# Optimization experiments

Hardware: AMD Instinct MI355X
Metric: run time of the kernel (lower is better)

Reference implementation:

```python
import jax, jax.numpy as jnp
import numpy as np
import math

B, T, D, H = 4, 2048, 2048, 16
HD = D // H  # 128


def rotate_half(x):
    half = x.shape[-1] // 2
    return jnp.concatenate([-x[..., half:], x[..., :half]], axis=-1)


def apply_rope(x, cos, sin):
    # x: [B,H,T,hd]; cos/sin: [T,hd] -> broadcast over B,H
    return x * cos[None, None] + rotate_half(x) * sin[None, None]


def setup_inputs() -> dict:
    key = jax.random.key(0)
    ks = jax.random.split(key, 6)
    x = jax.random.normal(ks[0], (B, T, D), dtype=jnp.float32)
    # standard RoPE tables
    inv_freq = 1.0 / (10000.0 ** (np.arange(0, HD, 2, dtype=np.float32) / HD))
    freqs = np.arange(T, dtype=np.float32)[:, None] * inv_freq[None, :]  # [T, hd/2]
    emb = np.concatenate([freqs, freqs], axis=-1)  # [T, hd]
    cos = jnp.asarray(np.cos(emb))
    sin = jnp.asarray(np.sin(emb))
    # additive causal mask [T,T]: 0 on/below diagonal, -1e9 above
    mask = jnp.where(jnp.tril(jnp.ones((T, T), dtype=bool)), 0.0, -1e9).astype(jnp.float32)
    scale = 0.02
    Wq = scale * jax.random.normal(ks[1], (D, D), dtype=jnp.float32)
    Wk = scale * jax.random.normal(ks[2], (D, D), dtype=jnp.float32)
    Wv = scale * jax.random.normal(ks[3], (D, D), dtype=jnp.float32)
    Wo = scale * jax.random.normal(ks[4], (D, D), dtype=jnp.float32)
    return {"x": x, "cos": cos, "sin": sin, "mask": mask,
            "Wq": Wq, "Wk": Wk, "Wv": Wv, "Wo": Wo}


def reference(x, cos, sin, mask, Wq, Wk, Wv, Wo):
    b, t, d = x.shape

    def split_heads(y):  # [B,T,D] -> [B,H,T,hd]
        return y.reshape(b, t, H, HD).transpose(0, 2, 1, 3)

    # nn.Linear: y = x @ W.T
    Q = apply_rope(split_heads(jnp.einsum('btd,od->bto', x, Wq)), cos, sin)
    K = apply_rope(split_heads(jnp.einsum('btd,od->bto', x, Wk)), cos, sin)
    V = split_heads(jnp.einsum('btd,od->bto', x, Wv))

    scores = jnp.einsum('bhqd,bhkd->bhqk', Q, K) / math.sqrt(HD)
    scores = scores + mask  # [T,T] broadcasts over [B,H,T,T]
    weights = jax.nn.softmax(scores, axis=-1)
    out = jnp.einsum('bhqk,bhkd->bhqd', weights, V)
    out = out.transpose(0, 2, 1, 3).reshape(b, t, d)
    return jnp.einsum('btd,od->bto', out, Wo)
```

## Files before the change

kernel.cpp:

```cpp
#include <hip/hip_runtime.h>
#include <hip/hip_bf16.h>

#define DEV static __device__ __forceinline__

typedef __attribute__((ext_vector_type(8))) _Float16 half8;
typedef __attribute__((ext_vector_type(4))) float f32x4;

constexpr int Bc = 4, Tc = 2048, Dc = 2048, Hc = 16;

DEV ushort f2h(float f) { _Float16 h = (_Float16)f; return __builtin_bit_cast(ushort, h); }
DEV float  h2f(ushort u) { return (float)__builtin_bit_cast(_Float16, u); }
DEV uint pk2h(float a, float b) {
  return __builtin_bit_cast(uint, __builtin_amdgcn_cvt_pkrtz(a, b));
}

DEV f32x4 MFMA(half8 a, half8 b, f32x4 c) {
  return __builtin_amdgcn_mfma_f32_16x16x32_f16(a, b, c, 0, 0, 0);
}

DEV void async_cp16(void* lds, const void* g) {
  __builtin_amdgcn_global_load_lds((const __attribute__((address_space(1))) void*)g,
                                   (__attribute__((address_space(3))) void*)lds,
                                   16, 0, 0);
}

__global__ __launch_bounds__(256) void cvtall(const float* __restrict__ x,
                                              const float* __restrict__ w0,
                                              const float* __restrict__ w1,
                                              const float* __restrict__ w2,
                                              const float* __restrict__ w3,
                                              ushort* __restrict__ xb,
                                              ushort* __restrict__ wb) {
  const int blk = (int)blockIdx.x;
  if (blk < 16384) {
    const int i = blk * 256 + (int)threadIdx.x;
    const float4 v = ((const float4*)x)[i];
    ushort4 o;
    o.x = f2h(v.x); o.y = f2h(v.y); o.z = f2h(v.z); o.w = f2h(v.w);
    ((ushort4*)xb)[i] = o;
    return;
  }
  const int wblk = blk - 16384;
  const int wsel = wblk >> 12;
  const int i = (wblk & 4095) * 256 + (int)threadIdx.x;
  const float* in = (wsel == 0) ? w0 : (wsel == 1) ? w1 : (wsel == 2) ? w2 : w3;
  const float4 v = ((const float4*)in)[i];
  ushort4 o;
  o.x = f2h(v.x); o.y = f2h(v.y); o.z = f2h(v.z); o.w = f2h(v.w);
  int row = i >> 9;
  const int cidx = i & 511;
  if (wsel < 2) {
    const int h = row >> 7, fr = row & 127;
    const int s_ = fr >> 6, j = fr & 63;
    row = h * 128 + (j >> 4) * 32 + s_ * 16 + (j & 15);
  }
  ((ushort4*)wb)[((size_t)wsel << 20) + row * 512 + cidx] = o;
}

__global__ __launch_bounds__(512, 2) void gemmqkv(const ushort* __restrict__ A,
                                                  const ushort* __restrict__ Bw,
                                                  ushort* __restrict__ Cq,
                                                  const float* __restrict__ cs,
                                                  const float* __restrict__ sn) {
  __shared__ ushort As[4][256 * 32];
  __shared__ ushort Bs[4][256 * 32];
  const int tid = threadIdx.x;
  const int lane = tid & 63, wid = tid >> 6;
  const int g = lane >> 4, q16 = lane & 15;
  const int wm = wid >> 2, wn = wid & 3;

  const int flat = (int)blockIdx.x;
  const int xcd = flat & 7, idx = flat >> 3;
  const int bm = xcd * 4 + (idx & 3);
  const int bn = idx >> 2;
  const ushort* Ab = A + (size_t)bm * 256 * Dc;
  const ushort* Bb = Bw + (size_t)bn * 256 * Dc;

#define STAGE1(KT, BUF, PH) do {                                               \
    const int pass_ = (PH) & 1;                                                \
    const int c_ = pass_ * 512 + tid;                                          \
    const int row_ = c_ >> 2, gl_ = c_ & 3;                                    \
    const int col_ = (KT) * 32 + ((gl_ ^ ((row_ >> 1) & 3)) << 3);             \
    if ((PH) < 2)                                                              \
      async_cp16(&As[BUF][(pass_ * 512 + wid * 64) * 8],                       \
                 Ab + (size_t)row_ * Dc + col_);                               \
    else                                                                       \
      async_cp16(&Bs[BUF][(pass_ * 512 + wid * 64) * 8],                       \
                 Bb + (size_t)row_ * Dc + col_);                               \
  } while (0)

  f32x4 acc[8][4] = {};

  for (int tt = 0; tt < 3; ++tt) {
    STAGE1(tt, tt, 0); STAGE1(tt, tt, 1);
    STAGE1(tt, tt, 2); STAGE1(tt, tt, 3);
  }

  const int sgz = (g ^ ((q16 >> 1) & 3)) << 3;

#pragma unroll 1
  for (int t = 0; t < 64; ++t) {
    const int sb = (t + 3) & 3;
    const bool st = (t + 3) < 64;
    const ushort* Asb = As[t & 3];
    const ushort* Bsb = Bs[t & 3];

    if (t + 2 < 64)      asm volatile("s_waitcnt vmcnt(8)" ::: "memory");
    else if (t + 1 < 64) asm volatile("s_waitcnt vmcnt(4)" ::: "memory");
    else                 asm volatile("s_waitcnt vmcnt(0)" ::: "memory");
    __builtin_amdgcn_s_barrier();
    __builtin_amdgcn_sched_barrier(0);

    half8 af0[4], af1[4], bf[4];
#pragma unroll
    for (int nf = 0; nf < 4; ++nf) {
      const int r = wn * 64 + nf * 16 + q16;
      bf[nf] = *(const half8*)&Bsb[r * 32 + sgz];
    }
#pragma unroll
    for (int mf = 0; mf < 4; ++mf) {
      const int r = wm * 128 + mf * 16 + q16;
      af0[mf] = *(const half8*)&Asb[r * 32 + sgz];
    }
#pragma unroll
    for (int mf = 0; mf < 4; ++mf) {
      const int r = wm * 128 + 64 + mf * 16 + q16;
      af1[mf] = *(const half8*)&Asb[r * 32 + sgz];
    }
    if (st) { STAGE1(t + 3, sb, 0); STAGE1(t + 3, sb, 1);
              STAGE1(t + 3, sb, 2); STAGE1(t + 3, sb, 3); }

    __builtin_amdgcn_s_setprio(1);
#pragma unroll
    for (int mf = 0; mf < 4; ++mf)
#pragma unroll
      for (int nf = 0; nf < 4; ++nf)
        acc[mf][nf] = MFMA(af0[mf], bf[nf], acc[mf][nf]);
#pragma unroll
    for (int mf = 0; mf < 4; ++mf)
#pragma unroll
      for (int nf = 0; nf < 4; ++nf)
        acc[4 + mf][nf] = MFMA(af1[mf], bf[nf], acc[4 + mf][nf]);
    __builtin_amdgcn_s_setprio(0);
  }
#undef STAGE1

  ushort* C = Cq + (size_t)(bn >> 3) * ((size_t)8192 * Dc);
  const int bn8 = bn & 7;
  const int m00 = bm * 256 + wm * 128 + g * 4;
  const int n0 = bn8 * 256 + wn * 64 + q16;

  if (bn < 16) {
#pragma unroll
    for (int mf = 0; mf < 8; ++mf)
#pragma unroll
      for (int p = 0; p < 2; ++p) {
        const int j = ((wn & 1) * 2 + p) * 16 + q16;
#pragma unroll
        for (int r = 0; r < 4; ++r) {
          const int m = m00 + mf * 16 + r;
          const int t = m & (Tc - 1);
          const float c = cs[t * 128 + j];
          const float s_ = sn[t * 128 + j];
          const float lo = acc[mf][2 * p][r];
          const float hi = acc[mf][2 * p + 1][r];
          C[(size_t)m * Dc + n0 + (2 * p) * 16] = f2h(lo * c - hi * s_);
          C[(size_t)m * Dc + n0 + (2 * p + 1) * 16] = f2h(hi * c + lo * s_);
        }
      }
  } else {
#pragma unroll
    for (int mf = 0; mf < 8; ++mf)
#pragma unroll
      for (int nf = 0; nf < 4; ++nf) {
        const int m0 = m00 + mf * 16;
        const int n = n0 + nf * 16;
#pragma unroll
        for (int r = 0; r < 4; ++r)
          C[(size_t)(m0 + r) * Dc + n] = f2h(acc[mf][nf][r]);
      }
  }
}

template <typename OutT>
__global__ __launch_bounds__(512, 2) void gemm256(const ushort* __restrict__ A,
                                                  const ushort* __restrict__ Bw,
                                                  OutT* __restrict__ C) {
  __shared__ ushort As[4][256 * 32];
  __shared__ ushort Bs[4][256 * 32];
  const int tid = threadIdx.x;
  const int lane = tid & 63, wid = tid >> 6;
  const int g = lane >> 4, q16 = lane & 15;
  const int wm = wid >> 2, wn = wid & 3;

  const int flat = (int)blockIdx.x;
  const int xcd = flat & 7, idx = flat >> 3;
  const int bm = xcd * 4 + (idx & 3);
  const int bn = idx >> 2;
  const ushort* Ab = A + (size_t)bm * 256 * Dc;
  const ushort* Bb = Bw + (size_t)bn * 256 * Dc;

#define STAGE1(KT, BUF, PH) do {                                               \
    const int pass_ = (PH) & 1;                                                \
    const int c_ = pass_ * 512 + tid;                                          \
    const int row_ = c_ >> 2, gl_ = c_ & 3;                                    \
    const int col_ = (KT) * 32 + ((gl_ ^ ((row_ >> 1) & 3)) << 3);             \
    if ((PH) < 2)                                                              \
      async_cp16(&As[BUF][(pass_ * 512 + wid * 64) * 8],                       \
                 Ab + (size_t)row_ * Dc + col_);                               \
    else                                                                       \
      async_cp16(&Bs[BUF][(pass_ * 512 + wid * 64) * 8],                       \
                 Bb + (size_t)row_ * Dc + col_);                               \
  } while (0)

  f32x4 acc[8][4] = {};

  for (int tt = 0; tt < 3; ++tt) {
    STAGE1(tt, tt, 0); STAGE1(tt, tt, 1);
    STAGE1(tt, tt, 2); STAGE1(tt, tt, 3);
  }

  const int sgz = (g ^ ((q16 >> 1) & 3)) << 3;

#pragma unroll 1
  for (int t = 0; t < 64; ++t) {
    const int sb = (t + 3) & 3;
    const bool st = (t + 3) < 64;
    const ushort* Asb = As[t & 3];
    const ushort* Bsb = Bs[t & 3];

    if (t + 2 < 64)      asm volatile("s_waitcnt vmcnt(8)" ::: "memory");
    else if (t + 1 < 64) asm volatile("s_waitcnt vmcnt(4)" ::: "memory");
    else                 asm volatile("s_waitcnt vmcnt(0)" ::: "memory");
    __builtin_amdgcn_s_barrier();
    __builtin_amdgcn_sched_barrier(0);

    half8 af0[4], af1[4], bf[4];
#pragma unroll
    for (int nf = 0; nf < 4; ++nf) {
      const int r = wn * 64 + nf * 16 + q16;
      bf[nf] = *(const half8*)&Bsb[r * 32 + sgz];
    }
#pragma unroll
    for (int mf = 0; mf < 4; ++mf) {
      const int r = wm * 128 + mf * 16 + q16;
      af0[mf] = *(const half8*)&Asb[r * 32 + sgz];
    }
#pragma unroll
    for (int mf = 0; mf < 4; ++mf) {
      const int r = wm * 128 + 64 + mf * 16 + q16;
      af1[mf] = *(const half8*)&Asb[r * 32 + sgz];
    }
    if (st) { STAGE1(t + 3, sb, 0); STAGE1(t + 3, sb, 1);
              STAGE1(t + 3, sb, 2); STAGE1(t + 3, sb, 3); }

    __builtin_amdgcn_s_setprio(1);
#pragma unroll
    for (int mf = 0; mf < 4; ++mf)
#pragma unroll
      for (int nf = 0; nf < 4; ++nf)
        acc[mf][nf] = MFMA(af0[mf], bf[nf], acc[mf][nf]);
#pragma unroll
    for (int mf = 0; mf < 4; ++mf)
#pragma unroll
      for (int nf = 0; nf < 4; ++nf)
        acc[4 + mf][nf] = MFMA(af1[mf], bf[nf], acc[4 + mf][nf]);
    __builtin_amdgcn_s_setprio(0);
  }
#undef STAGE1

  const int m00 = bm * 256 + wm * 128 + g * 4;
  const int n0 = bn * 256 + wn * 64 + q16;
#pragma unroll
  for (int mf = 0; mf < 8; ++mf)
#pragma unroll
    for (int nf = 0; nf < 4; ++nf) {
      const int m0 = m00 + mf * 16;
      const int n = n0 + nf * 16;
#pragma unroll
      for (int r = 0; r < 4; ++r) {
        const float v = acc[mf][nf][r];
        if constexpr (sizeof(OutT) == 2)
          C[(size_t)(m0 + r) * Dc + n] = (OutT)f2h(v);
        else
          C[(size_t)(m0 + r) * Dc + n] = (OutT)v;
      }
    }
}

__global__ __launch_bounds__(512, 2) void attn(const ushort* __restrict__ Q,
                                               const ushort* __restrict__ K,
                                               const ushort* __restrict__ V,
                                               ushort* __restrict__ O) {
  __shared__ ushort Ks[2][64 * 128];
  __shared__ ushort Vt[2][128 * 64];

  const int tid = threadIdx.x;
  const int lane = tid & 63, wid = tid >> 6;
  const int g = lane >> 4, q16 = lane & 15;

  const int flat = (int)(blockIdx.x + 4 * blockIdx.y);
  const int xcd = flat & 7, idx = flat >> 3;
  const int bh = xcd + 8 * (idx & 7);
  const int pr = idx >> 3;

  const int b = bh >> 4, h = bh & 15;
  const size_t headbase = ((size_t)b * Tc * Hc + h) * 128;
  const float SCL2 = 0.12751743f;

  const int vdc = (wid & 3) * 4 + (lane & 3);
  const int vkvp = (wid >> 2) * 16 + (lane >> 2);

  uint4 vreg[2];

#define ISSUEK(KT, BUF) do {                                                   \
    const ushort* Kb_ = K + headbase + (size_t)(KT) * 64 * Dc;                 \
    _Pragma("unroll") for (int i_ = 0; i_ < 2; ++i_) {                         \
      const int c_ = i_ * 512 + tid;                                           \
      const int kv_ = c_ >> 4, gl_ = c_ & 15;                                  \
      async_cp16(&Ks[BUF][(i_ * 512 + wid * 64) * 8],                          \
                 Kb_ + (size_t)kv_ * Dc + ((gl_ ^ (kv_ & 7)) << 3));           \
    }                                                                          \
  } while (0)

#define LOADV(KT) do {                                                         \
    const ushort* p0_ = V + headbase + (size_t)((KT) * 64 + 2 * vkvp) * Dc +   \
                        vdc * 8;                                               \
    vreg[0] = *(const uint4*)p0_;                                              \
    vreg[1] = *(const uint4*)(p0_ + Dc);                                       \
  } while (0)

#define WRITEV(BUF) do {                                                       \
    const ushort* e0_ = (const ushort*)&vreg[0];                               \
    const ushort* e1_ = (const ushort*)&vreg[1];                               \
    _Pragma("unroll") for (int j_ = 0; j_ < 8; ++j_) {                         \
      const int d_ = vdc * 8 + j_;                                             \
      const unsigned w_ = (unsigned)e0_[j_] | ((unsigned)e1_[j_] << 16);       \
      *(unsigned*)&Vt[BUF][(d_ * 64 + 2 * vkvp) ^ ((d_ & 7) << 3)] = w_;       \
    }                                                                          \
  } while (0)

#pragma unroll 1
  for (int half = 0; half < 2; ++half) {
    const int q0 = (half ? pr : 7 - pr) * 256;
    const int qrow = q0 + wid * 32;
    const int nt = q0 / 64 + 4;

    half8 qreg[2][4];
#pragma unroll
    for (int qf = 0; qf < 2; ++qf)
#pragma unroll
      for (int ds = 0; ds < 4; ++ds)
        qreg[qf][ds] = *(const half8*)(Q + headbase +
                       (size_t)(qrow + qf * 16 + q16) * Dc + ds * 32 + g * 8);

    f32x4 oacc[2][8] = {};
    float m_[2] = {-1e30f, -1e30f};
    float l_[2] = {0.f, 0.f};

    __builtin_amdgcn_s_barrier();
    __builtin_amdgcn_sched_barrier(0);
    ISSUEK(0, 0);
    LOADV(0);
    WRITEV(0);

#pragma unroll 1
    for (int kt = 0; kt < nt; ++kt) {
      const int cur = kt & 1;
      const int kv0 = kt * 64;
      asm volatile("s_waitcnt vmcnt(0) lgkmcnt(0)" ::: "memory");
      __builtin_amdgcn_s_barrier();
      __builtin_amdgcn_sched_barrier(0);
      if (kt + 1 < nt) {
        ISSUEK(kt + 1, cur ^ 1);
        LOADV(kt + 1);
      }

      if (kv0 <= qrow + 31) {
        const ushort* Ksb = Ks[cur];
        const ushort* Vtb = Vt[cur];
        f32x4 s[2][4] = {};
        __builtin_amdgcn_s_setprio(1);
#pragma unroll
        for (int ds = 0; ds < 4; ++ds) {
          half8 kf[4];
#pragma unroll
          for (int kvf = 0; kvf < 4; ++kvf) {
            const int kv = kvf * 16 + q16;
            kf[kvf] = *(const half8*)&Ksb[(kv * 128 + ds * 32 + g * 8) ^ ((kv & 7) << 3)];
          }
#pragma unroll
          for (int kvf = 0; kvf < 4; ++kvf)
#pragma unroll
            for (int qf = 0; qf < 2; ++qf)
              s[qf][kvf] = MFMA(kf[kvf], qreg[qf][ds], s[qf][kvf]);
        }
        __builtin_amdgcn_s_setprio(0);
        float pmax[2] = {-1e30f, -1e30f};
        if (kv0 + 63 > qrow) {
#pragma unroll
          for (int qf = 0; qf < 2; ++qf) {
            const int qg = qrow + qf * 16 + q16;
#pragma unroll
            for (int kvf = 0; kvf < 4; ++kvf)
#pragma unroll
              for (int r = 0; r < 4; ++r) {
                float v = s[qf][kvf][r];
                if ((kv0 + kvf * 16 + g * 4 + r) > qg) v = -1e30f;
                s[qf][kvf][r] = v;
                pmax[qf] = fmaxf(pmax[qf], v);
              }
          }
        } else {
#pragma unroll
          for (int qf = 0; qf < 2; ++qf)
#pragma unroll
            for (int kvf = 0; kvf < 4; ++kvf)
#pragma unroll
              for (int r = 0; r < 4; ++r)
                pmax[qf] = fmaxf(pmax[qf], s[qf][kvf][r]);
        }
#pragma unroll
        for (int qf = 0; qf < 2; ++qf) {
          pmax[qf] = fmaxf(pmax[qf], __shfl_xor(pmax[qf], 16));
          pmax[qf] = fmaxf(pmax[qf], __shfl_xor(pmax[qf], 32));
        }
        if (!__all((pmax[0] <= m_[0] + 16.f) & (pmax[1] <= m_[1] + 16.f))) {
#pragma unroll
          for (int qf = 0; qf < 2; ++qf) {
            const float mn2 = fmaxf(m_[qf], pmax[qf]);
            const float alpha = __builtin_exp2f((m_[qf] - mn2) * SCL2);
            m_[qf] = mn2;
            l_[qf] *= alpha;
#pragma unroll
            for (int df = 0; df < 8; ++df)
              oacc[qf][df] *= alpha;
          }
        }
        uint w[2][4][2];
#pragma unroll
        for (int qf = 0; qf < 2; ++qf) {
          const float mn = m_[qf];
          float lsum = 0.f;
#pragma unroll
          for (int kvf = 0; kvf < 4; ++kvf) {
            const float p0 = __builtin_exp2f((s[qf][kvf][0] - mn) * SCL2);
            const float p1 = __builtin_exp2f((s[qf][kvf][1] - mn) * SCL2);
            const float p2 = __builtin_exp2f((s[qf][kvf][2] - mn) * SCL2);
            const float p3 = __builtin_exp2f((s[qf][kvf][3] - mn) * SCL2);
            lsum += (p0 + p1) + (p2 + p3);
            w[qf][kvf][0] = pk2h(p0, p1);
            w[qf][kvf][1] = pk2h(p2, p3);
          }
          l_[qf] += lsum;
        }
        const bool ghi = g >= 2;
        const bool godd = (g & 1) != 0;
        half8 pb[2][2];
#pragma unroll
        for (int qf = 0; qf < 2; ++qf) {
          uint sA[2][2], sB[2][2];
#pragma unroll
          for (int c = 0; c < 2; ++c)
#pragma unroll
            for (int i = 0; i < 2; ++i) {
              sA[c][i] = ghi ? w[qf][2 * c + 1][i] : w[qf][2 * c][i];
              sB[c][i] = ghi ? w[qf][2 * c][i] : w[qf][2 * c + 1][i];
            }
          uint x16[2][2], x32[2][2], x48[2][2];
#pragma unroll
          for (int c = 0; c < 2; ++c)
#pragma unroll
            for (int i = 0; i < 2; ++i) {
              x16[c][i] = __shfl_xor(sA[c][i], 16);
              x32[c][i] = __shfl_xor(sB[c][i], 32);
              x48[c][i] = __shfl_xor(sB[c][i], 48);
            }
#pragma unroll
          for (int c = 0; c < 2; ++c) {
            uint4 t;
            t.x = godd ? (ghi ? x16[c][0] : x48[c][0]) : (ghi ? x32[c][0] : sA[c][0]);
            t.y = godd ? (ghi ? x16[c][1] : x48[c][1]) : (ghi ? x32[c][1] : sA[c][1]);
            t.z = godd ? (ghi ? sA[c][0] : x32[c][0]) : (ghi ? x48[c][0] : x16[c][0]);
            t.w = godd ? (ghi ? sA[c][1] : x32[c][1]) : (ghi ? x48[c][1] : x16[c][1]);
            pb[qf][c] = __builtin_bit_cast(half8, t);
          }
        }
        __builtin_amdgcn_s_setprio(1);
#pragma unroll
        for (int c = 0; c < 2; ++c) {
#pragma unroll
          for (int df = 0; df < 8; ++df) {
            const int d = df * 16 + q16;
            const half8 vf = *(const half8*)&Vtb[(d * 64 + c * 32 + g * 8) ^ ((d & 7) << 3)];
#pragma unroll
            for (int qf = 0; qf < 2; ++qf)
              oacc[qf][df] = MFMA(vf, pb[qf][c], oacc[qf][df]);
          }
        }
        __builtin_amdgcn_s_setprio(0);
      }

      if (kt + 1 < nt) WRITEV(cur ^ 1);
    }

#pragma unroll
    for (int qf = 0; qf < 2; ++qf) {
      float l = l_[qf];
      l += __shfl_xor(l, 16);
      l += __shfl_xor(l, 32);
      const float inv = 1.0f / l;
      const int t = qrow + qf * 16 + q16;
#pragma unroll
      for (int df = 0; df < 8; ++df) {
        const f32x4 v = oacc[qf][df];
        ushort4 o;
        o.x = f2h(v[0] * inv); o.y = f2h(v[1] * inv);
        o.z = f2h(v[2] * inv); o.w = f2h(v[3] * inv);
        *(ushort4*)(O + headbase + (size_t)t * Dc + df * 16 + g * 4) = o;
      }
    }
  }
#undef ISSUEK
#undef LOADV
#undef WRITEV
}

extern "C" void kernel_launch(void* const* d_in, const int* in_sizes, int n_in,
                              void* d_out, int out_size, void* d_ws, size_t ws_size,
                              hipStream_t stream) {
  (void)in_sizes; (void)n_in; (void)out_size; (void)ws_size;
  const float* x  = (const float*)d_in[0];
  const float* cs = (const float*)d_in[1];
  const float* sn = (const float*)d_in[2];
  const float* Wq = (const float*)d_in[4];
  const float* Wk = (const float*)d_in[5];
  const float* Wv = (const float*)d_in[6];
  const float* Wo = (const float*)d_in[7];
  float* out = (float*)d_out;

  char* ws = (char*)d_ws;
  const size_t MB = 1024 * 1024;
  ushort* xb  = (ushort*)(ws);
  ushort* wqb = (ushort*)(ws + 32 * MB);
  ushort* wob = (ushort*)(ws + 56 * MB);
  ushort* Qr  = (ushort*)(ws + 64 * MB);
  ushort* Kr  = (ushort*)(ws + 96 * MB);
  ushort* Vr  = (ushort*)(ws + 128 * MB);

  cvtall<<<32768, 256, 0, stream>>>(x, Wq, Wk, Wv, Wo, xb, wqb);

  gemmqkv<<<768, 512, 0, stream>>>(xb, wqb, Qr, cs, sn);

  attn<<<dim3(4, 64), 512, 0, stream>>>(Qr, Kr, Vr, xb);

  gemm256<float><<<256, 512, 0, stream>>>(xb, wob, out);
}
```

Baseline: 449.2 us.

## Switch GEMM mainloop to double-buffered BK=64 tiles with 8-way XOR swizzle

Both GEMM kernels (QKV projection and the generic 256x256 GEMM) change from a 4-stage BK=32 async pipeline to a 2-stage BK=64 pipeline. The LDS rows are now 64 halves wide with an 8-way XOR swizzle. Each iteration issues the next tile's loads up front, runs two k-substeps of MFMAs, then waits for all loads and barriers once. This halves the number of barriers and loop iterations. In exchange, prefetch depth drops to one tile and every iteration ends with a full vmcnt(0) wait, which can expose load latency.

```diff
diff --git a/kernel.cpp b/kernel.cpp
--- a/kernel.cpp
+++ b/kernel.cpp
@@ -62,8 +62,8 @@
                                                   ushort* __restrict__ Cq,
                                                   const float* __restrict__ cs,
                                                   const float* __restrict__ sn) {
-  __shared__ ushort As[4][256 * 32];
-  __shared__ ushort Bs[4][256 * 32];
+  __shared__ ushort As[2][256 * 64];
+  __shared__ ushort Bs[2][256 * 64];
   const int tid = threadIdx.x;
   const int lane = tid & 63, wid = tid >> 6;
   const int g = lane >> 4, q16 = lane & 15;
@@ -76,74 +76,87 @@
   const ushort* Ab = A + (size_t)bm * 256 * Dc;
   const ushort* Bb = Bw + (size_t)bn * 256 * Dc;
 
-#define STAGE1(KT, BUF, PH) do {                                               \
-    const int pass_ = (PH) & 1;                                                \
-    const int c_ = pass_ * 512 + tid;                                          \
-    const int row_ = c_ >> 2, gl_ = c_ & 3;                                    \
-    const int col_ = (KT) * 32 + ((gl_ ^ ((row_ >> 1) & 3)) << 3);             \
-    if ((PH) < 2)                                                              \
-      async_cp16(&As[BUF][(pass_ * 512 + wid * 64) * 8],                       \
+#define STAGE64(KT, BUF) do {                                                  \
+    _Pragma("unroll") for (int p_ = 0; p_ < 4; ++p_) {                         \
+      const int c_ = p_ * 512 + tid;                                           \
+      const int row_ = c_ >> 3, gl_ = c_ & 7;                                  \
+      const int col_ = (KT) * 64 + ((gl_ ^ (row_ & 7)) << 3);                  \
+      async_cp16(&As[BUF][(p_ * 512 + wid * 64) * 8],                          \
                  Ab + (size_t)row_ * Dc + col_);                               \
-    else                                                                       \
-      async_cp16(&Bs[BUF][(pass_ * 512 + wid * 64) * 8],                       \
+    }                                                                          \
+    _Pragma("unroll") for (int p_ = 0; p_ < 4; ++p_) {                         \
+      const int c_ = p_ * 512 + tid;                                           \
+      const int row_ = c_ >> 3, gl_ = c_ & 7;                                  \
+      const int col_ = (KT) * 64 + ((gl_ ^ (row_ & 7)) << 3);                  \
+      async_cp16(&Bs[BUF][(p_ * 512 + wid * 64) * 8],                          \
                  Bb + (size_t)row_ * Dc + col_);                               \
+    }                                                                          \
+  } while (0)
+
+#define READS64(BUF, KS) do {                                                  \
+    const ushort* Asb_ = As[BUF];                                              \
+    const ushort* Bsb_ = Bs[BUF];                                              \
+    _Pragma("unroll") for (int nf_ = 0; nf_ < 4; ++nf_) {                      \
+      const int r_ = wn * 64 + nf_ * 16 + q16;                                 \
+      bf[nf_] = *(const half8*)&Bsb_[r_ * 64 + ((((KS) * 4 + g) ^ (r_ & 7)) << 3)]; \
+    }                                                                          \
+    _Pragma("unroll") for (int mf_ = 0; mf_ < 4; ++mf_) {                      \
+      const int r_ = wm * 128 + mf_ * 16 + q16;                                \
+      af0[mf_] = *(const half8*)&Asb_[r_ * 64 + ((((KS) * 4 + g) ^ (r_ & 7)) << 3)]; \
+    }                                                                          \
+    _Pragma("unroll") for (int mf_ = 0; mf_ < 4; ++mf_) {                      \
+      const int r_ = wm * 128 + 64 + mf_ * 16 + q16;                           \
+      af1[mf_] = *(const half8*)&Asb_[r_ * 64 + ((((KS) * 4 + g) ^ (r_ & 7)) << 3)]; \
+    }                                                                          \
   } while (0)
 
   f32x4 acc[8][4] = {};
 
-  for (int tt = 0; tt < 3; ++tt) {
-    STAGE1(tt, tt, 0); STAGE1(tt, tt, 1);
-    STAGE1(tt, tt, 2); STAGE1(tt, tt, 3);
-  }
-
-  const int sgz = (g ^ ((q16 >> 1) & 3)) << 3;
+  STAGE64(0, 0);
+  asm volatile("s_waitcnt vmcnt(0)" ::: "memory");
+  __builtin_amdgcn_s_barrier();
+  __builtin_amdgcn_sched_barrier(0);
 
 #pragma unroll 1
-  for (int t = 0; t < 64; ++t) {
-    const int sb = (t + 3) & 3;
-    const bool st = (t + 3) < 64;
-    const ushort* Asb = As[t & 3];
-    const ushort* Bsb = Bs[t & 3];
-
-    if (t + 2 < 64)      asm volatile("s_waitcnt vmcnt(8)" ::: "memory");
-    else if (t + 1 < 64) asm volatile("s_waitcnt vmcnt(4)" ::: "memory");
-    else                 asm volatile("s_waitcnt vmcnt(0)" ::: "memory");
+  for (int t = 0; t < 32; ++t) {
+    const int rb = t & 1;
+    if (t + 1 < 32) STAGE64(t + 1, rb ^ 1);
+
+    half8 af0[4], af1[4], bf[4];
+    READS64(rb, 0);
+    __builtin_amdgcn_s_setprio(1);
+#pragma unroll
+    for (int mf = 0; mf < 4; ++mf)
+#pragma unroll
+      for (int nf = 0; nf < 4; ++nf)
+        acc[mf][nf] = MFMA(af0[mf], bf[nf], acc[mf][nf]);
+#pragma unroll
+    for (int mf = 0; mf < 4; ++mf)
+#pragma unroll
+      for (int nf = 0; nf < 4; ++nf)
+        acc[4 + mf][nf] = MFMA(af1[mf], bf[nf], acc[4 + mf][nf]);
+    __builtin_amdgcn_s_setprio(0);
+
+    READS64(rb, 1);
+    __builtin_amdgcn_s_setprio(1);
+#pragma unroll
+    for (int mf = 0; mf < 4; ++mf)
+#pragma unroll
+      for (int nf = 0; nf < 4; ++nf)
+        acc[mf][nf] = MFMA(af0[mf], bf[nf], acc[mf][nf]);
+#pragma unroll
+    for (int mf = 0; mf < 4; ++mf)
+#pragma unroll
+      for (int nf = 0; nf < 4; ++nf)
+        acc[4 + mf][nf] = MFMA(af1[mf], bf[nf], acc[4 + mf][nf]);
+    __builtin_amdgcn_s_setprio(0);
+
+    asm volatile("s_waitcnt vmcnt(0)" ::: "memory");
     __builtin_amdgcn_s_barrier();
     __builtin_amdgcn_sched_barrier(0);
-
-    half8 af0[4], af1[4], bf[4];
-#pragma unroll
-    for (int nf = 0; nf < 4; ++nf) {
-      const int r = wn * 64 + nf * 16 + q16;
-      bf[nf] = *(const half8*)&Bsb[r * 32 + sgz];
-    }
-#pragma unroll
-    for (int mf = 0; mf < 4; ++mf) {
-      const int r = wm * 128 + mf * 16 + q16;
-      af0[mf] = *(const half8*)&Asb[r * 32 + sgz];
-    }
-#pragma unroll
-    for (int mf = 0; mf < 4; ++mf) {
-      const int r = wm * 128 + 64 + mf * 16 + q16;
-      af1[mf] = *(const half8*)&Asb[r * 32 + sgz];
-    }
-    if (st) { STAGE1(t + 3, sb, 0); STAGE1(t + 3, sb, 1);
-              STAGE1(t + 3, sb, 2); STAGE1(t + 3, sb, 3); }
-
-    __builtin_amdgcn_s_setprio(1);
-#pragma unroll
-    for (int mf = 0; mf < 4; ++mf)
-#pragma unroll
-      for (int nf = 0; nf < 4; ++nf)
-        acc[mf][nf] = MFMA(af0[mf], bf[nf], acc[mf][nf]);
-#pragma unroll
-    for (int mf = 0; mf < 4; ++mf)
-#pragma unroll
-      for (int nf = 0; nf < 4; ++nf)
-        acc[4 + mf][nf] = MFMA(af1[mf], bf[nf], acc[4 + mf][nf]);
-    __builtin_amdgcn_s_setprio(0);
   }
-#undef STAGE1
+#undef READS64
+#undef STAGE64
 
   ushort* C = Cq + (size_t)(bn >> 3) * ((size_t)8192 * Dc);
   const int bn8 = bn & 7;
@@ -186,8 +199,8 @@
 __global__ __launch_bounds__(512, 2) void gemm256(const ushort* __restrict__ A,
                                                   const ushort* __restrict__ Bw,
                                                   OutT* __restrict__ C) {
-  __shared__ ushort As[4][256 * 32];
-  __shared__ ushort Bs[4][256 * 32];
+  __shared__ ushort As[2][256 * 64];
+  __shared__ ushort Bs[2][256 * 64];
   const int tid = threadIdx.x;
   const int lane = tid & 63, wid = tid >> 6;
   const int g = lane >> 4, q16 = lane & 15;
@@ -200,74 +213,87 @@
   const ushort* Ab = A + (size_t)bm * 256 * Dc;
   const ushort* Bb = Bw + (size_t)bn * 256 * Dc;
 
-#define STAGE1(KT, BUF, PH) do {                                               \
-    const int pass_ = (PH) & 1;                                                \
-    const int c_ = pass_ * 512 + tid;                                          \
-    const int row_ = c_ >> 2, gl_ = c_ & 3;                                    \
-    const int col_ = (KT) * 32 + ((gl_ ^ ((row_ >> 1) & 3)) << 3);             \
-    if ((PH) < 2)                                                              \
-      async_cp16(&As[BUF][(pass_ * 512 + wid * 64) * 8],                       \
+#define STAGE64(KT, BUF) do {                                                  \
+    _Pragma("unroll") for (int p_ = 0; p_ < 4; ++p_) {                         \
+      const int c_ = p_ * 512 + tid;                                           \
+      const int row_ = c_ >> 3, gl_ = c_ & 7;                                  \
+      const int col_ = (KT) * 64 + ((gl_ ^ (row_ & 7)) << 3);                  \
+      async_cp16(&As[BUF][(p_ * 512 + wid * 64) * 8],                          \
                  Ab + (size_t)row_ * Dc + col_);                               \
-    else                                                                       \
-      async_cp16(&Bs[BUF][(pass_ * 512 + wid * 64) * 8],                       \
+    }                                                                          \
+    _Pragma("unroll") for (int p_ = 0; p_ < 4; ++p_) {                         \
+      const int c_ = p_ * 512 + tid;                                           \
+      const int row_ = c_ >> 3, gl_ = c_ & 7;                                  \
+      const int col_ = (KT) * 64 + ((gl_ ^ (row_ & 7)) << 3);                  \
+      async_cp16(&Bs[BUF][(p_ * 512 + wid * 64) * 8],                          \
                  Bb + (size_t)row_ * Dc + col_);                               \
+    }                                                                          \
+  } while (0)
+
+#define READS64(BUF, KS) do {                                                  \
+    const ushort* Asb_ = As[BUF];                                              \
+    const ushort* Bsb_ = Bs[BUF];                                              \
+    _Pragma("unroll") for (int nf_ = 0; nf_ < 4; ++nf_) {                      \
+      const int r_ = wn * 64 + nf_ * 16 + q16;                                 \
+      bf[nf_] = *(const half8*)&Bsb_[r_ * 64 + ((((KS) * 4 + g) ^ (r_ & 7)) << 3)]; \
+    }                                                                          \
+    _Pragma("unroll") for (int mf_ = 0; mf_ < 4; ++mf_) {                      \
+      const int r_ = wm * 128 + mf_ * 16 + q16;                                \
+      af0[mf_] = *(const half8*)&Asb_[r_ * 64 + ((((KS) * 4 + g) ^ (r_ & 7)) << 3)]; \
+    }                                                                          \
+    _Pragma("unroll") for (int mf_ = 0; mf_ < 4; ++mf_) {                      \
+      const int r_ = wm * 128 + 64 + mf_ * 16 + q16;                           \
+      af1[mf_] = *(const half8*)&Asb_[r_ * 64 + ((((KS) * 4 + g) ^ (r_ & 7)) << 3)]; \
+    }                                                                          \
   } while (0)
 
   f32x4 acc[8][4] = {};
 
-  for (int tt = 0; tt < 3; ++tt) {
-    STAGE1(tt, tt, 0); STAGE1(tt, tt, 1);
-    STAGE1(tt, tt, 2); STAGE1(tt, tt, 3);
-  }
-
-  const int sgz = (g ^ ((q16 >> 1) & 3)) << 3;
+  STAGE64(0, 0);
+  asm volatile("s_waitcnt vmcnt(0)" ::: "memory");
+  __builtin_amdgcn_s_barrier();
+  __builtin_amdgcn_sched_barrier(0);
 
 #pragma unroll 1
-  for (int t = 0; t < 64; ++t) {
-    const int sb = (t + 3) & 3;
-    const bool st = (t + 3) < 64;
-    const ushort* Asb = As[t & 3];
-    const ushort* Bsb = Bs[t & 3];
-
-    if (t + 2 < 64)      asm volatile("s_waitcnt vmcnt(8)" ::: "memory");
-    else if (t + 1 < 64) asm volatile("s_waitcnt vmcnt(4)" ::: "memory");
-    else                 asm volatile("s_waitcnt vmcnt(0)" ::: "memory");
+  for (int t = 0; t < 32; ++t) {
+    const int rb = t & 1;
+    if (t + 1 < 32) STAGE64(t + 1, rb ^ 1);
+
+    half8 af0[4], af1[4], bf[4];
+    READS64(rb, 0);
+    __builtin_amdgcn_s_setprio(1);
+#pragma unroll
+    for (int mf = 0; mf < 4; ++mf)
+#pragma unroll
+      for (int nf = 0; nf < 4; ++nf)
+        acc[mf][nf] = MFMA(af0[mf], bf[nf], acc[mf][nf]);
+#pragma unroll
+    for (int mf = 0; mf < 4; ++mf)
+#pragma unroll
+      for (int nf = 0; nf < 4; ++nf)
+        acc[4 + mf][nf] = MFMA(af1[mf], bf[nf], acc[4 + mf][nf]);
+    __builtin_amdgcn_s_setprio(0);
+
+    READS64(rb, 1);
+    __builtin_amdgcn_s_setprio(1);
+#pragma unroll
+    for (int mf = 0; mf < 4; ++mf)
+#pragma unroll
+      for (int nf = 0; nf < 4; ++nf)
+        acc[mf][nf] = MFMA(af0[mf], bf[nf], acc[mf][nf]);
+#pragma unroll
+    for (int mf = 0; mf < 4; ++mf)
+#pragma unroll
+      for (int nf = 0; nf < 4; ++nf)
+        acc[4 + mf][nf] = MFMA(af1[mf], bf[nf], acc[4 + mf][nf]);
+    __builtin_amdgcn_s_setprio(0);
+
+    asm volatile("s_waitcnt vmcnt(0)" ::: "memory");
     __builtin_amdgcn_s_barrier();
     __builtin_amdgcn_sched_barrier(0);
-
-    half8 af0[4], af1[4], bf[4];
-#pragma unroll
-    for (int nf = 0; nf < 4; ++nf) {
-      const int r = wn * 64 + nf * 16 + q16;
-      bf[nf] = *(const half8*)&Bsb[r * 32 + sgz];
-    }
-#pragma unroll
-    for (int mf = 0; mf < 4; ++mf) {
-      const int r = wm * 128 + mf * 16 + q16;
-      af0[mf] = *(const half8*)&Asb[r * 32 + sgz];
-    }
-#pragma unroll
-    for (int mf = 0; mf < 4; ++mf) {
-      const int r = wm * 128 + 64 + mf * 16 + q16;
-      af1[mf] = *(const half8*)&Asb[r * 32 + sgz];
-    }
-    if (st) { STAGE1(t + 3, sb, 0); STAGE1(t + 3, sb, 1);
-              STAGE1(t + 3, sb, 2); STAGE1(t + 3, sb, 3); }
-
-    __builtin_amdgcn_s_setprio(1);
-#pragma unroll
-    for (int mf = 0; mf < 4; ++mf)
-#pragma unroll
-      for (int nf = 0; nf < 4; ++nf)
-        acc[mf][nf] = MFMA(af0[mf], bf[nf], acc[mf][nf]);
-#pragma unroll
-    for (int mf = 0; mf < 4; ++mf)
-#pragma unroll
-      for (int nf = 0; nf < 4; ++nf)
-        acc[4 + mf][nf] = MFMA(af1[mf], bf[nf], acc[4 + mf][nf]);
-    __builtin_amdgcn_s_setprio(0);
   }
-#undef STAGE1
+#undef READS64
+#undef STAGE64
 
   const int m00 = bm * 256 + wm * 128 + g * 4;
   const int n0 = bn * 256 + wn * 64 + q16;
```

Measured after the change: 454.7 us. About the same (+1.2%).
